# Kernel tuning notes

Hardware: AMD Instinct MI355X
Metric: run time of the kernel (lower is better)

## Reference

```python
import jax, jax.numpy as jnp
import numpy as np

B, S = 4, 1024          # sequences, tokens per sequence (equal-length prefill)
T = B * S               # total ragged tokens
H, D = 16, 128          # heads, head_size
HID = H * D             # hidden_size = 2048
THETA = 10000.0


def setup_inputs() -> dict:
    key = jax.random.key(0)
    k0, k1, k2, k3 = jax.random.split(key, 4)
    hidden_states = jax.random.normal(k0, (T, HID), jnp.float32) * 0.02
    # real RoPE tables (PositionRotaryEmbedding.static), [T, D//2]
    inv_freq = 1.0 / (THETA ** (jnp.arange(0, D, 2, dtype=jnp.float32) / D))
    pos = jnp.tile(jnp.arange(S, dtype=jnp.float32), B)  # position resets per sequence
    ang = pos[:, None] * inv_freq[None, :]
    cos, sin = jnp.cos(ang), jnp.sin(ang)
    w_attn = jax.random.normal(k1, (3 * HID, HID), jnp.float32) * 0.02
    b_attn = jax.random.normal(k2, (3 * HID,), jnp.float32) * 0.02
    w_proj = jax.random.normal(k3, (HID, HID), jnp.float32) * 0.02
    cu_seqlens = (jnp.arange(B + 1, dtype=jnp.int32) * S)
    return {"hidden_states": hidden_states, "cos": cos, "sin": sin,
            "w_attn": w_attn, "b_attn": b_attn, "w_proj": w_proj,
            "cu_seqlens": cu_seqlens}


def _rope(x, cos, sin):
    # x: [T, H, D]; cos/sin: [T, D//2]; rotate-half (neox) style
    x1, x2 = jnp.split(x, 2, axis=-1)
    c, s = cos[:, None, :], sin[:, None, :]
    return jnp.concatenate([x1 * c - x2 * s, x2 * c + x1 * s], axis=-1)


def reference(hidden_states, cos, sin, w_attn, b_attn, w_proj, cu_seqlens):
    scale = D ** -0.5
    qkv = hidden_states @ w_attn.T + b_attn          # [T, 3*HID]
    q = qkv[:, :HID].reshape(T, H, D)
    k = qkv[:, HID:2 * HID].reshape(T, H, D)
    v = qkv[:, 2 * HID:].reshape(T, H, D)
    q = _rope(q, cos, sin)
    k = _rope(k, cos, sin)
    # equal-length ragged batch -> [B, S, H, D]; causal flash-attn (prefill path)
    qb = q.reshape(B, S, H, D)
    kb = k.reshape(B, S, H, D)
    vb = v.reshape(B, S, H, D)
    scores = jnp.einsum('bqhd,bkhd->bhqk', qb, kb) * scale
    causal = jnp.tril(jnp.ones((S, S), dtype=bool))
    scores = jnp.where(causal[None, None], scores, jnp.finfo(scores.dtype).min)
    p = jax.nn.softmax(scores, axis=-1)
    o = jnp.einsum('bhqk,bkhd->bqhd', p, vb).reshape(T, HID)
    return o @ w_proj.T                               # c_proj, no bias
```

## Files before the change

### kernel.cpp

```cpp
#include <hip/hip_runtime.h>

typedef __bf16 bf16x8 __attribute__((ext_vector_type(8)));
typedef __bf16 bf16x4 __attribute__((ext_vector_type(4)));
typedef float  f32x4  __attribute__((ext_vector_type(4)));

#define T_TOT 4096
#define SEQ   1024
#define BATCH 4
#define HEADS 16
#define DIM   128
#define HIDN  2048
#define QKVW  6144

__device__ __forceinline__ void gld_lds16(const void* g, void* l) {
  __builtin_amdgcn_global_load_lds(
      (const __attribute__((address_space(1))) unsigned int*)g,
      (__attribute__((address_space(3))) unsigned int*)l, 16, 0, 0);
}

__global__ void f2b_all(const float* __restrict__ h,  __bf16* __restrict__ oh,
                        const float* __restrict__ wa, __bf16* __restrict__ owa,
                        const float* __restrict__ wp, __bf16* __restrict__ owp)
{
  const int bid = blockIdx.x;
  const float* in;
  __bf16* out;
  int base;
  if (bid < 8192)       { in = h;  out = oh;  base = bid; }
  else if (bid < 20480) { in = wa; out = owa; base = bid - 8192; }
  else                  { in = wp; out = owp; base = bid - 20480; }
  const int i = (base * 256 + threadIdx.x) * 4;
  const float4 v = *(const float4*)(in + i);
  bf16x4 o;
  o[0] = (__bf16)v.x; o[1] = (__bf16)v.y; o[2] = (__bf16)v.z; o[3] = (__bf16)v.w;
  *(bf16x4*)(out + i) = o;
}

template<int BIAS, typename OUT_T>
__global__ __launch_bounds__(256, 2) void gemm_wide(
    const __bf16* __restrict__ A, int lda,
    const __bf16* __restrict__ B, int ldb,
    const float* __restrict__ bias,
    OUT_T* __restrict__ C, int ldc, int K, int nby)
{
  __shared__ __bf16 sA[3 * 256 * 32];
  __shared__ __bf16 sB[3 * 128 * 32];
  const int tid = threadIdx.x;
  const int w = tid >> 6, lane = tid & 63;
  const int lq = lane & 15, lg = lane >> 4;
  const int wm = w >> 1, wn = w & 1;

  const int nwg = gridDim.x, cpx = nwg >> 3, bid = blockIdx.x;
  const int wgid = (bid & 7) * cpx + (bid >> 3);
  const int by = wgid % nby, bx = wgid / nby;
  const int bm = by * 256, bn = bx * 128;

  const int srow = tid >> 2;
  const int scol = ((tid & 3) ^ ((srow >> 1) & 3)) * 8;
  const __bf16* gA = A + (size_t)(bm + srow) * lda + scol;
  const __bf16* gB = B + (size_t)(bn + srow) * ldb + scol;
  __bf16* dA = &sA[w * 512];
  __bf16* dB = &sB[w * 512];

  const int NT = K >> 5;

#define STAGE(t, bf) {                                               \
    const __bf16* sa_ = gA + (size_t)(t) * 32;                       \
    gld_lds16(sa_,                      dA + (bf) * 8192);           \
    gld_lds16(sa_ + (size_t) 64 * lda,  dA + (bf) * 8192 + 2048);    \
    gld_lds16(sa_ + (size_t)128 * lda,  dA + (bf) * 8192 + 4096);    \
    gld_lds16(sa_ + (size_t)192 * lda,  dA + (bf) * 8192 + 6144);    \
    const __bf16* sb_ = gB + (size_t)(t) * 32;                       \
    gld_lds16(sb_,                      dB + (bf) * 4096);           \
    gld_lds16(sb_ + (size_t) 64 * ldb,  dB + (bf) * 4096 + 2048); }

  f32x4 acc[8][4] = {};

  const int colo = (lg ^ ((lq >> 1) & 3)) * 8;
  const int offA = (wm * 128 + lq) * 32 + colo;
  const int offB = (wn * 64 + lq) * 32 + colo;

  STAGE(0, 0); STAGE(1, 1);
  asm volatile("s_waitcnt vmcnt(6)" ::: "memory");
  __builtin_amdgcn_s_barrier();
  asm volatile("" ::: "memory");

  bf16x8 a[8], b[4];
  {
    const __bf16* pA = &sA[offA];
    const __bf16* pB = &sB[offB];
#pragma unroll
    for (int m = 0; m < 8; ++m) a[m] = *(const bf16x8*)(pA + m * 512);
#pragma unroll
    for (int n = 0; n < 4; ++n) b[n] = *(const bf16x8*)(pB + n * 512);
  }

  int bcur = 0;
  for (int t = 0; t < NT; ++t) {
    int bstg = bcur + 2; if (bstg >= 3) bstg -= 3;
    const bool st = (t + 2) < NT;
    if (st) STAGE(t + 2, bstg);

    asm volatile("s_waitcnt lgkmcnt(0)" ::: "memory");
    __builtin_amdgcn_sched_barrier(0);
    __builtin_amdgcn_s_setprio(1);
#pragma unroll
    for (int m = 0; m < 8; ++m)
#pragma unroll
      for (int n = 0; n < 4; ++n)
        acc[m][n] = __builtin_amdgcn_mfma_f32_16x16x32_bf16(a[m], b[n], acc[m][n], 0, 0, 0);
    __builtin_amdgcn_s_setprio(0);

    if (t + 1 < NT) {
      if (st) { asm volatile("s_waitcnt vmcnt(6)" ::: "memory"); }
      else    { asm volatile("s_waitcnt vmcnt(0)" ::: "memory"); }
      __builtin_amdgcn_s_barrier();
      asm volatile("" ::: "memory");
      const int bnext = (bcur + 1 == 3) ? 0 : bcur + 1;
      const __bf16* pA = &sA[bnext * 8192 + offA];
      const __bf16* pB = &sB[bnext * 4096 + offB];
#pragma unroll
      for (int m = 0; m < 8; ++m) a[m] = *(const bf16x8*)(pA + m * 512);
#pragma unroll
      for (int n = 0; n < 4; ++n) b[n] = *(const bf16x8*)(pB + n * 512);
    }
    bcur = (bcur + 1 == 3) ? 0 : bcur + 1;
  }
#undef STAGE

#pragma unroll
  for (int n = 0; n < 4; ++n) {
    const int col = bn + wn * 64 + n * 16 + lq;
    const float bv = BIAS ? bias[col] : 0.0f;
#pragma unroll
    for (int m = 0; m < 8; ++m)
#pragma unroll
      for (int r = 0; r < 4; ++r) {
        const int row = bm + wm * 128 + m * 16 + lg * 4 + r;
        C[(size_t)row * ldc + col] = (OUT_T)(acc[m][n][r] + bv);
      }
  }
}

template<int BIAS, typename OUT_T>
__global__ __launch_bounds__(256, 3) void gemm_sq(
    const __bf16* __restrict__ A, int lda,
    const __bf16* __restrict__ B, int ldb,
    const float* __restrict__ bias,
    OUT_T* __restrict__ C, int ldc, int K, int nby)
{
  __shared__ __bf16 sA[3 * 128 * 32];
  __shared__ __bf16 sB[3 * 128 * 32];
  const int tid = threadIdx.x;
  const int w = tid >> 6, lane = tid & 63;
  const int lq = lane & 15, lg = lane >> 4;
  const int wm = w >> 1, wn = w & 1;

  const int nwg = gridDim.x, cpx = nwg >> 3, bid = blockIdx.x;
  const int wgid = (bid & 7) * cpx + (bid >> 3);
  const int by = wgid % nby, bx = wgid / nby;
  const int bm = by * 128, bn = bx * 128;

  const int srow = tid >> 2;
  const int scol = ((tid & 3) ^ ((srow >> 1) & 3)) * 8;
  const __bf16* gA = A + (size_t)(bm + srow) * lda + scol;
  const __bf16* gB = B + (size_t)(bn + srow) * ldb + scol;
  const int w16 = w * 16;
  const int NT = K >> 5;

#define STAGE(t, bf) {                                                    \
    const __bf16* sa_ = gA + (size_t)(t) * 32;                            \
    gld_lds16(sa_,                     &sA[(bf) * 4096 + (w16) * 32]);    \
    gld_lds16(sa_ + (size_t)64 * lda,  &sA[(bf) * 4096 + (64 + w16) * 32]); \
    const __bf16* sb_ = gB + (size_t)(t) * 32;                            \
    gld_lds16(sb_,                     &sB[(bf) * 4096 + (w16) * 32]);    \
    gld_lds16(sb_ + (size_t)64 * ldb,  &sB[(bf) * 4096 + (64 + w16) * 32]); }

  f32x4 acc[4][4] = {};

  const int colo = (lg ^ ((lq >> 1) & 3)) * 8;
  const int offA = (wm * 64 + lq) * 32 + colo;
  const int offB = (wn * 64 + lq) * 32 + colo;

  STAGE(0, 0); STAGE(1, 1);
  asm volatile("s_waitcnt vmcnt(4)" ::: "memory");
  __builtin_amdgcn_s_barrier();
  asm volatile("" ::: "memory");

  bf16x8 a[4], b[4];
  {
    const __bf16* pA = &sA[offA];
    const __bf16* pB = &sB[offB];
#pragma unroll
    for (int m = 0; m < 4; ++m) a[m] = *(const bf16x8*)(pA + m * 512);
#pragma unroll
    for (int n = 0; n < 4; ++n) b[n] = *(const bf16x8*)(pB + n * 512);
  }

  int bcur = 0;
  for (int t = 0; t < NT; ++t) {
    int bstg = bcur + 2; if (bstg >= 3) bstg -= 3;
    const bool st = (t + 2) < NT;
    if (st) STAGE(t + 2, bstg);

    asm volatile("s_waitcnt lgkmcnt(0)" ::: "memory");
    __builtin_amdgcn_sched_barrier(0);
    __builtin_amdgcn_s_setprio(1);
#pragma unroll
    for (int m = 0; m < 4; ++m)
#pragma unroll
      for (int n = 0; n < 4; ++n)
        acc[m][n] = __builtin_amdgcn_mfma_f32_16x16x32_bf16(a[m], b[n], acc[m][n], 0, 0, 0);
    __builtin_amdgcn_s_setprio(0);

    if (t + 1 < NT) {
      if (st) { asm volatile("s_waitcnt vmcnt(4)" ::: "memory"); }
      else    { asm volatile("s_waitcnt vmcnt(0)" ::: "memory"); }
      __builtin_amdgcn_s_barrier();
      asm volatile("" ::: "memory");
      const int bnext = (bcur + 1 == 3) ? 0 : bcur + 1;
      const __bf16* pA = &sA[bnext * 4096 + offA];
      const __bf16* pB = &sB[bnext * 4096 + offB];
#pragma unroll
      for (int m = 0; m < 4; ++m) a[m] = *(const bf16x8*)(pA + m * 512);
#pragma unroll
      for (int n = 0; n < 4; ++n) b[n] = *(const bf16x8*)(pB + n * 512);
    }
    bcur = (bcur + 1 == 3) ? 0 : bcur + 1;
  }
#undef STAGE

#pragma unroll
  for (int n = 0; n < 4; ++n) {
    const int col = bn + wn * 64 + n * 16 + lq;
    const float bv = BIAS ? bias[col] : 0.0f;
#pragma unroll
    for (int m = 0; m < 4; ++m)
#pragma unroll
      for (int r = 0; r < 4; ++r) {
        const int row = bm + wm * 64 + m * 16 + lg * 4 + r;
        C[(size_t)row * ldc + col] = (OUT_T)(acc[m][n][r] + bv);
      }
  }
}

__global__ __launch_bounds__(256) void pack_kernel(const __bf16* __restrict__ qkv,
                                                   const float* __restrict__ cosb,
                                                   const float* __restrict__ sinb,
                                                   __bf16* __restrict__ Qp,
                                                   __bf16* __restrict__ Kp,
                                                   __bf16* __restrict__ Vt)
{
  __shared__ __bf16 tile[64][136];
  const int bh = blockIdx.y, b = bh >> 4, h = bh & 15;
  const int s0 = blockIdx.x * 64;
  const int tid = threadIdx.x;
  const int j0 = (tid & 7) * 8;
  const float qsc = 0.08838834764831845f;

#pragma unroll
  for (int it = 0; it < 2; ++it) {
    const int r = (tid >> 3) + it * 32;
    const int s = s0 + r;
    const size_t t = (size_t)b * SEQ + s;
    float cc[8], ss[8];
    *(float4*)&cc[0] = *(const float4*)&cosb[t * 64 + j0];
    *(float4*)&cc[4] = *(const float4*)&cosb[t * 64 + j0 + 4];
    *(float4*)&ss[0] = *(const float4*)&sinb[t * 64 + j0];
    *(float4*)&ss[4] = *(const float4*)&sinb[t * 64 + j0 + 4];
    const __bf16* src = qkv + t * QKVW + h * DIM;
    const bf16x8 q1 = *(const bf16x8*)(src + j0);
    const bf16x8 q2 = *(const bf16x8*)(src + 64 + j0);
    const bf16x8 k1 = *(const bf16x8*)(src + HIDN + j0);
    const bf16x8 k2 = *(const bf16x8*)(src + HIDN + 64 + j0);
    bf16x8 oq1, oq2, ok1, ok2;
#pragma unroll
    for (int jj = 0; jj < 8; ++jj) {
      const float c = cc[jj], sn = ss[jj];
      const float a1 = (float)q1[jj], a2 = (float)q2[jj];
      const float b1 = (float)k1[jj], b2 = (float)k2[jj];
      oq1[jj] = (__bf16)((a1 * c - a2 * sn) * qsc);
      oq2[jj] = (__bf16)((a2 * c + a1 * sn) * qsc);
      ok1[jj] = (__bf16)(b1 * c - b2 * sn);
      ok2[jj] = (__bf16)(b2 * c + b1 * sn);
    }
    __bf16* dq = Qp + ((size_t)bh * SEQ + s) * DIM + j0;
    __bf16* dk = Kp + ((size_t)bh * SEQ + s) * DIM + j0;
    *(bf16x8*)dq = oq1; *(bf16x8*)(dq + 64) = oq2;
    *(bf16x8*)dk = ok1; *(bf16x8*)(dk + 64) = ok2;
  }

#pragma unroll
  for (int i = 0; i < 4; ++i) {
    const int r = (tid >> 4) + i * 16;
    const int c = (tid & 15) * 8;
    *(bf16x8*)&tile[r][c] =
        *(const bf16x8*)&qkv[((size_t)b * SEQ + s0 + r) * QKVW + 2 * HIDN + h * DIM + c];
  }
  __syncthreads();
#pragma unroll
  for (int i = 0; i < 4; ++i) {
    const int d = (tid >> 3) + i * 32;
    const int scc = (tid & 7) * 8;
    bf16x8 v;
#pragma unroll
    for (int jj = 0; jj < 8; ++jj) v[jj] = tile[scc + jj][d];
    *(bf16x8*)&Vt[((size_t)bh * DIM + d) * SEQ + s0 + scc] = v;
  }
}

__global__ __launch_bounds__(256, 2) void attn_kernel(const __bf16* __restrict__ Qp,
                                                      const __bf16* __restrict__ Kp,
                                                      const __bf16* __restrict__ Vt,
                                                      __bf16* __restrict__ O)
{
  __shared__ __bf16 sK[2][64 * 128];
  __shared__ __bf16 sV[2][128 * 64];
  __shared__ __bf16 sP[4][32 * 64];
  const int w = threadIdx.x >> 6, lane = threadIdx.x & 63;
  const int lq = lane & 15, lg = lane >> 4;
  const int bh = blockIdx.y, b = bh >> 4, h = bh & 15;
  const int qb = ((int)blockIdx.x + bh) & 7;
  const int q0 = qb * 128 + w * 32;
  const int NTb = 2 * qb + 2;
  const int kend = q0 + 32;

  const __bf16* Qh = Qp + (size_t)bh * SEQ * DIM;
  const __bf16* Kh = Kp + (size_t)bh * SEQ * DIM;
  const __bf16* Vh = Vt + (size_t)bh * DIM * SEQ;

  const int krow = lane >> 4;
  const int kgr  = lane & 15;
  const int vrow = lane >> 3;
  const int vgr  = lane & 7;
  const __bf16* Vsrc = Vh + (size_t)(w * 32 + vrow) * SEQ + (vgr ^ vrow) * 8;

  auto ASTAGE = [&](int ktn, int p) {
#pragma unroll
    for (int i = 0; i < 4; ++i) {
      const int rb = w * 16 + i * 4;
      gld_lds16(Kh + (size_t)(ktn + rb + krow) * DIM + (kgr ^ (i * 4 + krow)) * 8,
                &sK[p][rb * DIM]);
    }
#pragma unroll
    for (int i = 0; i < 4; ++i) {
      gld_lds16(Vsrc + (size_t)i * 8 * SEQ + ktn, &sV[p][(w * 32 + i * 8) * 64]);
    }
  };

  bf16x8 aq[2][4];
#pragma unroll
  for (int m = 0; m < 2; ++m)
#pragma unroll
    for (int kk = 0; kk < 4; ++kk)
      aq[m][kk] = *(const bf16x8*)(Qh + (size_t)(q0 + m * 16 + lq) * DIM + kk * 32 + lg * 8);

  f32x4 accO[2][8] = {};
  float mrow[2][4], lrow[2][4];
#pragma unroll
  for (int m = 0; m < 2; ++m)
#pragma unroll
    for (int r = 0; r < 4; ++r) { mrow[m][r] = -1e30f; lrow[m][r] = 0.0f; }

  ASTAGE(0, 0);
  asm volatile("s_waitcnt vmcnt(0)" ::: "memory");
  __builtin_amdgcn_s_barrier();

  int p = 0;
  for (int t = 0; t < NTb; ++t) {
    const int kt = t * 64;
    if (t + 1 < NTb) ASTAGE(kt + 64, p ^ 1);

    if (kt < kend) {
      f32x4 s[2][4] = {};
#pragma unroll
      for (int n = 0; n < 4; ++n) {
        const int rowb = (n * 16 + lq) * DIM;
#pragma unroll
        for (int kk = 0; kk < 4; ++kk) {
          const bf16x8 bk = *(const bf16x8*)&sK[p][rowb + ((4 * kk + lg) ^ lq) * 8];
#pragma unroll
          for (int m = 0; m < 2; ++m)
            s[m][n] = __builtin_amdgcn_mfma_f32_16x16x32_bf16(aq[m][kk], bk, s[m][n], 0, 0, 0);
        }
      }
      if (kt + 63 > q0) {
#pragma unroll
        for (int n = 0; n < 4; ++n) {
          const int kpos = kt + n * 16 + lq;
#pragma unroll
          for (int m = 0; m < 2; ++m)
#pragma unroll
            for (int r = 0; r < 4; ++r)
              if (kpos > q0 + m * 16 + lg * 4 + r) s[m][n][r] = -1e30f;
        }
      }
#pragma unroll
      for (int m = 0; m < 2; ++m) {
#pragma unroll
        for (int r = 0; r < 4; ++r) {
          float mx = fmaxf(fmaxf(s[m][0][r], s[m][1][r]), fmaxf(s[m][2][r], s[m][3][r]));
          mx = fmaxf(mx, __shfl_xor(mx, 1));
          mx = fmaxf(mx, __shfl_xor(mx, 2));
          mx = fmaxf(mx, __shfl_xor(mx, 4));
          mx = fmaxf(mx, __shfl_xor(mx, 8));
          const float mnew = fmaxf(mrow[m][r], mx);
          const float alpha = __expf(mrow[m][r] - mnew);
          mrow[m][r] = mnew;
          float rs = 0.0f;
#pragma unroll
          for (int n = 0; n < 4; ++n) {
            const float pv = __expf(s[m][n][r] - mnew);
            s[m][n][r] = pv;
            rs += pv;
          }
          rs += __shfl_xor(rs, 1); rs += __shfl_xor(rs, 2);
          rs += __shfl_xor(rs, 4); rs += __shfl_xor(rs, 8);
          lrow[m][r] = lrow[m][r] * alpha + rs;
#pragma unroll
          for (int f = 0; f < 8; ++f) accO[m][f][r] *= alpha;
        }
      }
#pragma unroll
      for (int m = 0; m < 2; ++m)
#pragma unroll
        for (int n = 0; n < 4; ++n)
#pragma unroll
          for (int r = 0; r < 4; ++r) {
            const int prow = m * 16 + lg * 4 + r;
            const int cb = (n * 16 + lq) * 2;
            const int addr = prow * 128 + (((cb >> 4) ^ (prow & 7)) << 4) + (cb & 15);
            *(__bf16*)((char*)&sP[w][0] + addr) = (__bf16)s[m][n][r];
          }
      asm volatile("s_waitcnt lgkmcnt(0)" ::: "memory");
#pragma unroll
      for (int kk2 = 0; kk2 < 2; ++kk2) {
        bf16x8 ap[2];
#pragma unroll
        for (int m = 0; m < 2; ++m) {
          const int prow = m * 16 + lq;
          ap[m] = *(const bf16x8*)((char*)&sP[w][0] +
                   prow * 128 + (((4 * kk2 + lg) ^ (lq & 7)) << 4));
        }
#pragma unroll
        for (int f = 0; f < 8; ++f) {
          const bf16x8 bv = *(const bf16x8*)&sV[p][(f * 16 + lq) * 64 +
                                                   ((4 * kk2 + lg) ^ (lq & 7)) * 8];
#pragma unroll
          for (int m = 0; m < 2; ++m)
            accO[m][f] = __builtin_amdgcn_mfma_f32_16x16x32_bf16(ap[m], bv, accO[m][f], 0, 0, 0);
        }
      }
    }
    asm volatile("s_waitcnt vmcnt(0)" ::: "memory");
    __builtin_amdgcn_s_barrier();
    p ^= 1;
  }

#pragma unroll
  for (int m = 0; m < 2; ++m)
#pragma unroll
    for (int f = 0; f < 8; ++f)
#pragma unroll
      for (int r = 0; r < 4; ++r) {
        const float v = accO[m][f][r] / lrow[m][r];
        O[((size_t)b * SEQ + q0 + m * 16 + lg * 4 + r) * HIDN + h * DIM + f * 16 + lq] = (__bf16)v;
      }
}

extern "C" void kernel_launch(void* const* d_in, const int* in_sizes, int n_in,
                              void* d_out, int out_size, void* d_ws, size_t ws_size,
                              hipStream_t stream)
{
  const float* hidden = (const float*)d_in[0];
  const float* cosb   = (const float*)d_in[1];
  const float* sinb   = (const float*)d_in[2];
  const float* w_attn = (const float*)d_in[3];
  const float* b_attn = (const float*)d_in[4];
  const float* w_proj = (const float*)d_in[5];

  char* ws = (char*)d_ws;
  __bf16* hid_bf   = (__bf16*)(ws);
  __bf16* wattn_bf = (__bf16*)(ws + 16777216);
  __bf16* wproj_bf = (__bf16*)(ws + 41943040);
  __bf16* qkv      = (__bf16*)(ws + 50331648);
  __bf16* Qp       = (__bf16*)(ws);
  __bf16* Kp       = (__bf16*)(ws + 16777216);
  __bf16* Vt       = (__bf16*)(ws + 100663296);
  __bf16* Obuf     = (__bf16*)(ws + 117440512);
  float* out = (float*)d_out;

  f2b_all<<<24576, 256, 0, stream>>>(hidden, hid_bf, w_attn, wattn_bf, w_proj, wproj_bf);

  gemm_wide<1, __bf16><<<768, 256, 0, stream>>>(
      hid_bf, HIDN, wattn_bf, HIDN, b_attn, qkv, QKVW, HIDN, 16);

  pack_kernel<<<dim3(16, 64), 256, 0, stream>>>(qkv, cosb, sinb, Qp, Kp, Vt);
  attn_kernel<<<dim3(8, 64), 256, 0, stream>>>(Qp, Kp, Vt, Obuf);

  gemm_sq<0, float><<<512, 256, 0, stream>>>(
      Obuf, HIDN, wproj_bf, HIDN, nullptr, out, HIDN, HIDN, 32);
}
```

Before: 270.0 us.

## Load GEMM B operand directly from global into registers, bypassing LDS

Both GEMM kernels stop staging the weight (B) tile through shared memory. Each wave now loads its B fragments straight from global memory into registers, double-buffered two iterations ahead, while A keeps the triple-buffered LDS pipeline. This halves LDS traffic and LDS footprint, with vmcnt wait counts retuned to match the extra outstanding loads. The cost is more register pressure, and the B loads from global are redundant across the waves that share a column and less coalesced.

```diff
diff --git a/kernel.cpp b/kernel.cpp
--- a/kernel.cpp
+++ b/kernel.cpp
@@ -37,14 +37,13 @@
 }
 
 template<int BIAS, typename OUT_T>
-__global__ __launch_bounds__(256, 2) void gemm_wide(
+__global__ __launch_bounds__(256, 2) void gemm_hyb(
     const __bf16* __restrict__ A, int lda,
     const __bf16* __restrict__ B, int ldb,
     const float* __restrict__ bias,
     OUT_T* __restrict__ C, int ldc, int K, int nby)
 {
   __shared__ __bf16 sA[3 * 256 * 32];
-  __shared__ __bf16 sB[3 * 128 * 32];
   const int tid = threadIdx.x;
   const int w = tid >> 6, lane = tid & 63;
   const int lq = lane & 15, lg = lane >> 4;
@@ -58,75 +57,83 @@
   const int srow = tid >> 2;
   const int scol = ((tid & 3) ^ ((srow >> 1) & 3)) * 8;
   const __bf16* gA = A + (size_t)(bm + srow) * lda + scol;
-  const __bf16* gB = B + (size_t)(bn + srow) * ldb + scol;
   __bf16* dA = &sA[w * 512];
-  __bf16* dB = &sB[w * 512];
+
+  const __bf16* gBf = B + (size_t)(bn + wn * 64 + lq) * ldb + lg * 8;
 
   const int NT = K >> 5;
 
-#define STAGE(t, bf) {                                               \
+#define STAGEA(t, bf) {                                              \
     const __bf16* sa_ = gA + (size_t)(t) * 32;                       \
     gld_lds16(sa_,                      dA + (bf) * 8192);           \
     gld_lds16(sa_ + (size_t) 64 * lda,  dA + (bf) * 8192 + 2048);    \
     gld_lds16(sa_ + (size_t)128 * lda,  dA + (bf) * 8192 + 4096);    \
-    gld_lds16(sa_ + (size_t)192 * lda,  dA + (bf) * 8192 + 6144);    \
-    const __bf16* sb_ = gB + (size_t)(t) * 32;                       \
-    gld_lds16(sb_,                      dB + (bf) * 4096);           \
-    gld_lds16(sb_ + (size_t) 64 * ldb,  dB + (bf) * 4096 + 2048); }
+    gld_lds16(sa_ + (size_t)192 * lda,  dA + (bf) * 8192 + 6144); }
+
+#define BLOAD(t, breg) {                                             \
+    const __bf16* pb_ = gBf + (size_t)(t) * 32;                      \
+    breg[0] = *(const bf16x8*)(pb_);                                 \
+    breg[1] = *(const bf16x8*)(pb_ + (size_t)16 * ldb);              \
+    breg[2] = *(const bf16x8*)(pb_ + (size_t)32 * ldb);              \
+    breg[3] = *(const bf16x8*)(pb_ + (size_t)48 * ldb); }
 
   f32x4 acc[8][4] = {};
+  bf16x8 a[8], bA[4], bB[4];
 
   const int colo = (lg ^ ((lq >> 1) & 3)) * 8;
   const int offA = (wm * 128 + lq) * 32 + colo;
-  const int offB = (wn * 64 + lq) * 32 + colo;
-
-  STAGE(0, 0); STAGE(1, 1);
-  asm volatile("s_waitcnt vmcnt(6)" ::: "memory");
+
+  BLOAD(0, bA);
+  STAGEA(0, 0);
+  BLOAD(1, bB);
+  STAGEA(1, 1);
+  asm volatile("s_waitcnt vmcnt(8)" ::: "memory");
   __builtin_amdgcn_s_barrier();
   asm volatile("" ::: "memory");
-
-  bf16x8 a[8], b[4];
   {
     const __bf16* pA = &sA[offA];
-    const __bf16* pB = &sB[offB];
 #pragma unroll
     for (int m = 0; m < 8; ++m) a[m] = *(const bf16x8*)(pA + m * 512);
-#pragma unroll
-    for (int n = 0; n < 4; ++n) b[n] = *(const bf16x8*)(pB + n * 512);
-  }
-
-  int bcur = 0;
-  for (int t = 0; t < NT; ++t) {
-    int bstg = bcur + 2; if (bstg >= 3) bstg -= 3;
-    const bool st = (t + 2) < NT;
-    if (st) STAGE(t + 2, bstg);
-
-    asm volatile("s_waitcnt lgkmcnt(0)" ::: "memory");
-    __builtin_amdgcn_sched_barrier(0);
-    __builtin_amdgcn_s_setprio(1);
-#pragma unroll
-    for (int m = 0; m < 8; ++m)
-#pragma unroll
-      for (int n = 0; n < 4; ++n)
-        acc[m][n] = __builtin_amdgcn_mfma_f32_16x16x32_bf16(a[m], b[n], acc[m][n], 0, 0, 0);
-    __builtin_amdgcn_s_setprio(0);
-
-    if (t + 1 < NT) {
-      if (st) { asm volatile("s_waitcnt vmcnt(6)" ::: "memory"); }
-      else    { asm volatile("s_waitcnt vmcnt(0)" ::: "memory"); }
-      __builtin_amdgcn_s_barrier();
-      asm volatile("" ::: "memory");
-      const int bnext = (bcur + 1 == 3) ? 0 : bcur + 1;
-      const __bf16* pA = &sA[bnext * 8192 + offA];
-      const __bf16* pB = &sB[bnext * 4096 + offB];
-#pragma unroll
-      for (int m = 0; m < 8; ++m) a[m] = *(const bf16x8*)(pA + m * 512);
-#pragma unroll
-      for (int n = 0; n < 4; ++n) b[n] = *(const bf16x8*)(pB + n * 512);
-    }
-    bcur = (bcur + 1 == 3) ? 0 : bcur + 1;
-  }
-#undef STAGE
+  }
+
+  int bcurA = 0;
+
+#define ITER(t, bth, WVM) {                                                   \
+    int bstg = bcurA + 2; if (bstg >= 3) bstg -= 3;                           \
+    const bool st = (t + 2) < NT;                                             \
+    if (st) STAGEA(t + 2, bstg);                                              \
+    asm volatile("s_waitcnt lgkmcnt(0)" ::: "memory");                        \
+    __builtin_amdgcn_sched_barrier(0);                                        \
+    __builtin_amdgcn_s_setprio(1);                                            \
+    _Pragma("unroll")                                                         \
+    for (int m = 0; m < 8; ++m)                                               \
+      _Pragma("unroll")                                                       \
+      for (int n = 0; n < 4; ++n)                                             \
+        acc[m][n] = __builtin_amdgcn_mfma_f32_16x16x32_bf16(a[m], bth[n],     \
+                                                            acc[m][n], 0,0,0);\
+    __builtin_amdgcn_s_setprio(0);                                            \
+    if (st) BLOAD(t + 2, bth);                                                \
+    if (t + 1 < NT) {                                                         \
+      if (st) { asm volatile("s_waitcnt vmcnt(" #WVM ")" ::: "memory"); }     \
+      else    { asm volatile("s_waitcnt vmcnt(4)"  ::: "memory"); }           \
+      __builtin_amdgcn_s_barrier();                                           \
+      asm volatile("" ::: "memory");                                          \
+      const int bnx = (bcurA + 1 == 3) ? 0 : bcurA + 1;                       \
+      const __bf16* pA = &sA[bnx * 8192 + offA];                              \
+      _Pragma("unroll")                                                       \
+      for (int m = 0; m < 8; ++m) a[m] = *(const bf16x8*)(pA + m * 512);      \
+    }                                                                         \
+    bcurA = (bcurA + 1 == 3) ? 0 : bcurA + 1; }
+
+  ITER(0, bA, 8);
+  ITER(1, bB, 12);
+  for (int t = 2; t < NT; t += 2) {
+    ITER(t,     bA, 12);
+    ITER(t + 1, bB, 12);
+  }
+#undef ITER
+#undef STAGEA
+#undef BLOAD
 
 #pragma unroll
   for (int n = 0; n < 4; ++n) {
@@ -143,14 +150,13 @@
 }
 
 template<int BIAS, typename OUT_T>
-__global__ __launch_bounds__(256, 3) void gemm_sq(
+__global__ __launch_bounds__(256, 3) void gemm_sqh(
     const __bf16* __restrict__ A, int lda,
     const __bf16* __restrict__ B, int ldb,
     const float* __restrict__ bias,
     OUT_T* __restrict__ C, int ldc, int K, int nby)
 {
   __shared__ __bf16 sA[3 * 128 * 32];
-  __shared__ __bf16 sB[3 * 128 * 32];
   const int tid = threadIdx.x;
   const int w = tid >> 6, lane = tid & 63;
   const int lq = lane & 15, lg = lane >> 4;
@@ -164,71 +170,81 @@
   const int srow = tid >> 2;
   const int scol = ((tid & 3) ^ ((srow >> 1) & 3)) * 8;
   const __bf16* gA = A + (size_t)(bm + srow) * lda + scol;
-  const __bf16* gB = B + (size_t)(bn + srow) * ldb + scol;
   const int w16 = w * 16;
+
+  const __bf16* gBf = B + (size_t)(bn + wn * 64 + lq) * ldb + lg * 8;
+
   const int NT = K >> 5;
 
-#define STAGE(t, bf) {                                                    \
-    const __bf16* sa_ = gA + (size_t)(t) * 32;                            \
-    gld_lds16(sa_,                     &sA[(bf) * 4096 + (w16) * 32]);    \
-    gld_lds16(sa_ + (size_t)64 * lda,  &sA[(bf) * 4096 + (64 + w16) * 32]); \
-    const __bf16* sb_ = gB + (size_t)(t) * 32;                            \
-    gld_lds16(sb_,                     &sB[(bf) * 4096 + (w16) * 32]);    \
-    gld_lds16(sb_ + (size_t)64 * ldb,  &sB[(bf) * 4096 + (64 + w16) * 32]); }
+#define STAGEA(t, bf) {                                                     \
+    const __bf16* sa_ = gA + (size_t)(t) * 32;                              \
+    gld_lds16(sa_,                     &sA[(bf) * 4096 + (w16) * 32]);      \
+    gld_lds16(sa_ + (size_t)64 * lda,  &sA[(bf) * 4096 + (64 + w16) * 32]); }
+
+#define BLOAD(t, breg) {                                             \
+    const __bf16* pb_ = gBf + (size_t)(t) * 32;                      \
+    breg[0] = *(const bf16x8*)(pb_);                                 \
+    breg[1] = *(const bf16x8*)(pb_ + (size_t)16 * ldb);              \
+    breg[2] = *(const bf16x8*)(pb_ + (size_t)32 * ldb);              \
+    breg[3] = *(const bf16x8*)(pb_ + (size_t)48 * ldb); }
 
   f32x4 acc[4][4] = {};
+  bf16x8 a[4], bA[4], bB[4];
 
   const int colo = (lg ^ ((lq >> 1) & 3)) * 8;
   const int offA = (wm * 64 + lq) * 32 + colo;
-  const int offB = (wn * 64 + lq) * 32 + colo;
-
-  STAGE(0, 0); STAGE(1, 1);
-  asm volatile("s_waitcnt vmcnt(4)" ::: "memory");
+
+  BLOAD(0, bA);
+  STAGEA(0, 0);
+  BLOAD(1, bB);
+  STAGEA(1, 1);
+  asm volatile("s_waitcnt vmcnt(6)" ::: "memory");
   __builtin_amdgcn_s_barrier();
   asm volatile("" ::: "memory");
-
-  bf16x8 a[4], b[4];
   {
     const __bf16* pA = &sA[offA];
-    const __bf16* pB = &sB[offB];
 #pragma unroll
     for (int m = 0; m < 4; ++m) a[m] = *(const bf16x8*)(pA + m * 512);
-#pragma unroll
-    for (int n = 0; n < 4; ++n) b[n] = *(const bf16x8*)(pB + n * 512);
-  }
-
-  int bcur = 0;
-  for (int t = 0; t < NT; ++t) {
-    int bstg = bcur + 2; if (bstg >= 3) bstg -= 3;
-    const bool st = (t + 2) < NT;
-    if (st) STAGE(t + 2, bstg);
-
-    asm volatile("s_waitcnt lgkmcnt(0)" ::: "memory");
-    __builtin_amdgcn_sched_barrier(0);
-    __builtin_amdgcn_s_setprio(1);
-#pragma unroll
-    for (int m = 0; m < 4; ++m)
-#pragma unroll
-      for (int n = 0; n < 4; ++n)
-        acc[m][n] = __builtin_amdgcn_mfma_f32_16x16x32_bf16(a[m], b[n], acc[m][n], 0, 0, 0);
-    __builtin_amdgcn_s_setprio(0);
-
-    if (t + 1 < NT) {
-      if (st) { asm volatile("s_waitcnt vmcnt(4)" ::: "memory"); }
-      else    { asm volatile("s_waitcnt vmcnt(0)" ::: "memory"); }
-      __builtin_amdgcn_s_barrier();
-      asm volatile("" ::: "memory");
-      const int bnext = (bcur + 1 == 3) ? 0 : bcur + 1;
-      const __bf16* pA = &sA[bnext * 4096 + offA];
-      const __bf16* pB = &sB[bnext * 4096 + offB];
-#pragma unroll
-      for (int m = 0; m < 4; ++m) a[m] = *(const bf16x8*)(pA + m * 512);
-#pragma unroll
-      for (int n = 0; n < 4; ++n) b[n] = *(const bf16x8*)(pB + n * 512);
-    }
-    bcur = (bcur + 1 == 3) ? 0 : bcur + 1;
-  }
-#undef STAGE
+  }
+
+  int bcurA = 0;
+
+#define ITER(t, bth, WVM) {                                                   \
+    int bstg = bcurA + 2; if (bstg >= 3) bstg -= 3;                           \
+    const bool st = (t + 2) < NT;                                             \
+    if (st) STAGEA(t + 2, bstg);                                              \
+    asm volatile("s_waitcnt lgkmcnt(0)" ::: "memory");                        \
+    __builtin_amdgcn_sched_barrier(0);                                        \
+    __builtin_amdgcn_s_setprio(1);                                            \
+    _Pragma("unroll")                                                         \
+    for (int m = 0; m < 4; ++m)                                               \
+      _Pragma("unroll")                                                       \
+      for (int n = 0; n < 4; ++n)                                             \
+        acc[m][n] = __builtin_amdgcn_mfma_f32_16x16x32_bf16(a[m], bth[n],     \
+                                                            acc[m][n], 0,0,0);\
+    __builtin_amdgcn_s_setprio(0);                                            \
+    if (st) BLOAD(t + 2, bth);                                                \
+    if (t + 1 < NT) {                                                         \
+      if (st) { asm volatile("s_waitcnt vmcnt(" #WVM ")" ::: "memory"); }     \
+      else    { asm volatile("s_waitcnt vmcnt(2)"  ::: "memory"); }           \
+      __builtin_amdgcn_s_barrier();                                           \
+      asm volatile("" ::: "memory");                                          \
+      const int bnx = (bcurA + 1 == 3) ? 0 : bcurA + 1;                       \
+      const __bf16* pA = &sA[bnx * 4096 + offA];                              \
+      _Pragma("unroll")                                                       \
+      for (int m = 0; m < 4; ++m) a[m] = *(const bf16x8*)(pA + m * 512);      \
+    }                                                                         \
+    bcurA = (bcurA + 1 == 3) ? 0 : bcurA + 1; }
+
+  ITER(0, bA, 6);
+  ITER(1, bB, 10);
+  for (int t = 2; t < NT; t += 2) {
+    ITER(t,     bA, 10);
+    ITER(t + 1, bB, 10);
+  }
+#undef ITER
+#undef STAGEA
+#undef BLOAD
 
 #pragma unroll
   for (int n = 0; n < 4; ++n) {
@@ -492,12 +508,12 @@
 
   f2b_all<<<24576, 256, 0, stream>>>(hidden, hid_bf, w_attn, wattn_bf, w_proj, wproj_bf);
 
-  gemm_wide<1, __bf16><<<768, 256, 0, stream>>>(
+  gemm_hyb<1, __bf16><<<768, 256, 0, stream>>>(
       hid_bf, HIDN, wattn_bf, HIDN, b_attn, qkv, QKVW, HIDN, 16);
 
   pack_kernel<<<dim3(16, 64), 256, 0, stream>>>(qkv, cosb, sinb, Qp, Kp, Vt);
   attn_kernel<<<dim3(8, 64), 256, 0, stream>>>(Qp, Kp, Vt, Obuf);
 
-  gemm_sq<0, float><<<512, 256, 0, stream>>>(
+  gemm_sqh<0, float><<<512, 256, 0, stream>>>(
       Obuf, HIDN, wproj_bf, HIDN, nullptr, out, HIDN, HIDN, 32);
 }
```

Result: slower. 338.6 us (+25.4%).

## Fuse RoPE, Q scaling and V transpose into QKV GEMM epilogue

Applied to the files above, without the earlier changes.

The separate pack kernel is removed. The QKV GEMM epilogue now writes Q and K directly in per-head layout with RoPE applied, exchanging rotate-half partners between the two wn waves through LDS scratch. It also writes V transposed directly. This drops the round trip of the intermediate qkv buffer and one kernel launch. In exchange the epilogue gains extra barriers, scattered 2-byte stores and per-element cos/sin loads, which may be poorly coalesced.

```diff
diff --git a/kernel.cpp b/kernel.cpp
--- a/kernel.cpp
+++ b/kernel.cpp
@@ -36,15 +36,19 @@
   *(bf16x4*)(out + i) = o;
 }
 
-template<int BIAS, typename OUT_T>
-__global__ __launch_bounds__(256, 2) void gemm_wide(
-    const __bf16* __restrict__ A, int lda,
-    const __bf16* __restrict__ B, int ldb,
+__global__ __launch_bounds__(256, 2) void gemm_qkv(
+    const __bf16* __restrict__ A,
+    const __bf16* __restrict__ B,
     const float* __restrict__ bias,
-    OUT_T* __restrict__ C, int ldc, int K, int nby)
+    const float* __restrict__ cosb,
+    const float* __restrict__ sinb,
+    __bf16* __restrict__ Qp,
+    __bf16* __restrict__ Kp,
+    __bf16* __restrict__ Vt)
 {
   __shared__ __bf16 sA[3 * 256 * 32];
   __shared__ __bf16 sB[3 * 128 * 32];
+  const int lda = HIDN, ldb = HIDN;
   const int tid = threadIdx.x;
   const int w = tid >> 6, lane = tid & 63;
   const int lq = lane & 15, lg = lane >> 4;
@@ -52,7 +56,7 @@
 
   const int nwg = gridDim.x, cpx = nwg >> 3, bid = blockIdx.x;
   const int wgid = (bid & 7) * cpx + (bid >> 3);
-  const int by = wgid % nby, bx = wgid / nby;
+  const int by = wgid % 16, bx = wgid / 16;
   const int bm = by * 256, bn = bx * 128;
 
   const int srow = tid >> 2;
@@ -62,7 +66,7 @@
   __bf16* dA = &sA[w * 512];
   __bf16* dB = &sB[w * 512];
 
-  const int NT = K >> 5;
+  const int NT = HIDN >> 5;
 
 #define STAGE(t, bf) {                                               \
     const __bf16* sa_ = gA + (size_t)(t) * 32;                       \
@@ -128,17 +132,57 @@
   }
 #undef STAGE
 
-#pragma unroll
-  for (int n = 0; n < 4; ++n) {
-    const int col = bn + wn * 64 + n * 16 + lq;
-    const float bv = BIAS ? bias[col] : 0.0f;
-#pragma unroll
-    for (int m = 0; m < 8; ++m)
-#pragma unroll
-      for (int r = 0; r < 4; ++r) {
-        const int row = bm + wm * 128 + m * 16 + lg * 4 + r;
-        C[(size_t)row * ldc + col] = (OUT_T)(acc[m][n][r] + bv);
-      }
+  const int region = bx >> 4;
+  const int h = bx & 15;
+  if (region == 2) {
+#pragma unroll
+    for (int n = 0; n < 4; ++n) {
+      const int col = bn + wn * 64 + n * 16 + lq;
+      const int d = wn * 64 + n * 16 + lq;
+      const float bv = bias[col];
+#pragma unroll
+      for (int m = 0; m < 8; ++m) {
+        const int row = bm + wm * 128 + m * 16 + lg * 4;
+        const int b_ = row >> 10, s0 = row & 1023;
+        bf16x4 o;
+#pragma unroll
+        for (int r = 0; r < 4; ++r) o[r] = (__bf16)(acc[m][n][r] + bv);
+        *(bf16x4*)&Vt[((size_t)(b_ * 16 + h) * 128 + d) * 1024 + s0] = o;
+      }
+    }
+  } else {
+    __bf16* scr = sA;
+    __bf16* Dst = region ? Kp : Qp;
+    const float qs = region ? 1.0f : 0.08838834764831845f;
+    __syncthreads();
+#pragma unroll
+    for (int n = 0; n < 4; ++n) {
+      const int j = n * 16 + lq;
+      const float bv = bias[bn + wn * 64 + j];
+#pragma unroll
+      for (int m = 0; m < 8; ++m)
+#pragma unroll
+        for (int r = 0; r < 4; ++r) {
+          const int rl = wm * 128 + m * 16 + lg * 4 + r;
+          scr[(wn * 256 + rl) * 16 + lq] = (__bf16)(acc[m][n][r] + bv);
+        }
+      __syncthreads();
+#pragma unroll
+      for (int m = 0; m < 8; ++m)
+#pragma unroll
+        for (int r = 0; r < 4; ++r) {
+          const int rl = wm * 128 + m * 16 + lg * 4 + r;
+          const int t = bm + rl;
+          const float own = acc[m][n][r] + bv;
+          const float prt = (float)scr[((wn ^ 1) * 256 + rl) * 16 + lq];
+          const float c  = cosb[(size_t)t * 64 + j];
+          const float sn = sinb[(size_t)t * 64 + j];
+          const float o = (wn == 0 ? own * c - prt * sn : own * c + prt * sn) * qs;
+          const int b_ = t >> 10, s = t & 1023;
+          Dst[((size_t)(b_ * 16 + h) * 1024 + s) * 128 + wn * 64 + j] = (__bf16)o;
+        }
+      __syncthreads();
+    }
   }
 }
 
@@ -241,71 +285,6 @@
         const int row = bm + wm * 64 + m * 16 + lg * 4 + r;
         C[(size_t)row * ldc + col] = (OUT_T)(acc[m][n][r] + bv);
       }
-  }
-}
-
-__global__ __launch_bounds__(256) void pack_kernel(const __bf16* __restrict__ qkv,
-                                                   const float* __restrict__ cosb,
-                                                   const float* __restrict__ sinb,
-                                                   __bf16* __restrict__ Qp,
-                                                   __bf16* __restrict__ Kp,
-                                                   __bf16* __restrict__ Vt)
-{
-  __shared__ __bf16 tile[64][136];
-  const int bh = blockIdx.y, b = bh >> 4, h = bh & 15;
-  const int s0 = blockIdx.x * 64;
-  const int tid = threadIdx.x;
-  const int j0 = (tid & 7) * 8;
-  const float qsc = 0.08838834764831845f;
-
-#pragma unroll
-  for (int it = 0; it < 2; ++it) {
-    const int r = (tid >> 3) + it * 32;
-    const int s = s0 + r;
-    const size_t t = (size_t)b * SEQ + s;
-    float cc[8], ss[8];
-    *(float4*)&cc[0] = *(const float4*)&cosb[t * 64 + j0];
-    *(float4*)&cc[4] = *(const float4*)&cosb[t * 64 + j0 + 4];
-    *(float4*)&ss[0] = *(const float4*)&sinb[t * 64 + j0];
-    *(float4*)&ss[4] = *(const float4*)&sinb[t * 64 + j0 + 4];
-    const __bf16* src = qkv + t * QKVW + h * DIM;
-    const bf16x8 q1 = *(const bf16x8*)(src + j0);
-    const bf16x8 q2 = *(const bf16x8*)(src + 64 + j0);
-    const bf16x8 k1 = *(const bf16x8*)(src + HIDN + j0);
-    const bf16x8 k2 = *(const bf16x8*)(src + HIDN + 64 + j0);
-    bf16x8 oq1, oq2, ok1, ok2;
-#pragma unroll
-    for (int jj = 0; jj < 8; ++jj) {
-      const float c = cc[jj], sn = ss[jj];
-      const float a1 = (float)q1[jj], a2 = (float)q2[jj];
-      const float b1 = (float)k1[jj], b2 = (float)k2[jj];
-      oq1[jj] = (__bf16)((a1 * c - a2 * sn) * qsc);
-      oq2[jj] = (__bf16)((a2 * c + a1 * sn) * qsc);
-      ok1[jj] = (__bf16)(b1 * c - b2 * sn);
-      ok2[jj] = (__bf16)(b2 * c + b1 * sn);
-    }
-    __bf16* dq = Qp + ((size_t)bh * SEQ + s) * DIM + j0;
-    __bf16* dk = Kp + ((size_t)bh * SEQ + s) * DIM + j0;
-    *(bf16x8*)dq = oq1; *(bf16x8*)(dq + 64) = oq2;
-    *(bf16x8*)dk = ok1; *(bf16x8*)(dk + 64) = ok2;
-  }
-
-#pragma unroll
-  for (int i = 0; i < 4; ++i) {
-    const int r = (tid >> 4) + i * 16;
-    const int c = (tid & 15) * 8;
-    *(bf16x8*)&tile[r][c] =
-        *(const bf16x8*)&qkv[((size_t)b * SEQ + s0 + r) * QKVW + 2 * HIDN + h * DIM + c];
-  }
-  __syncthreads();
-#pragma unroll
-  for (int i = 0; i < 4; ++i) {
-    const int d = (tid >> 3) + i * 32;
-    const int scc = (tid & 7) * 8;
-    bf16x8 v;
-#pragma unroll
-    for (int jj = 0; jj < 8; ++jj) v[jj] = tile[scc + jj][d];
-    *(bf16x8*)&Vt[((size_t)bh * DIM + d) * SEQ + s0 + scc] = v;
   }
 }
 
@@ -483,19 +462,17 @@
   __bf16* hid_bf   = (__bf16*)(ws);
   __bf16* wattn_bf = (__bf16*)(ws + 16777216);
   __bf16* wproj_bf = (__bf16*)(ws + 41943040);
-  __bf16* qkv      = (__bf16*)(ws + 50331648);
-  __bf16* Qp       = (__bf16*)(ws);
-  __bf16* Kp       = (__bf16*)(ws + 16777216);
-  __bf16* Vt       = (__bf16*)(ws + 100663296);
-  __bf16* Obuf     = (__bf16*)(ws + 117440512);
+  __bf16* Qp       = (__bf16*)(ws + 50331648);
+  __bf16* Kp       = (__bf16*)(ws + 67108864);
+  __bf16* Vt       = (__bf16*)(ws + 83886080);
+  __bf16* Obuf     = (__bf16*)(ws + 100663296);
   float* out = (float*)d_out;
 
   f2b_all<<<24576, 256, 0, stream>>>(hidden, hid_bf, w_attn, wattn_bf, w_proj, wproj_bf);
 
-  gemm_wide<1, __bf16><<<768, 256, 0, stream>>>(
-      hid_bf, HIDN, wattn_bf, HIDN, b_attn, qkv, QKVW, HIDN, 16);
-
-  pack_kernel<<<dim3(16, 64), 256, 0, stream>>>(qkv, cosb, sinb, Qp, Kp, Vt);
+  gemm_qkv<<<768, 256, 0, stream>>>(
+      hid_bf, wattn_bf, b_attn, cosb, sinb, Qp, Kp, Vt);
+
   attn_kernel<<<dim3(8, 64), 256, 0, stream>>>(Qp, Kp, Vt, Obuf);
 
   gemm_sq<0, float><<<512, 256, 0, stream>>>(
```

Result: slower. 429.9 us (+59.2%).
